# Performance work log

Hardware: AMD Instinct MI355X
Metric: run time of the kernel (lower is better)

## Reference

```python
import jax, jax.numpy as jnp
import numpy as np

N = 12288      # num nodes == in_num_dim (num_center_nodes)
D_IN = 512     # in_node_dim
D_EMB = 128    # embed_dim
D_OUT = 64     # out_dim
E = 393216     # num edges (avg degree 32)
NEG_SLOPE = 0.2  # GATConv default negative_slope


def _glorot(k, shape):
    lim = float(np.sqrt(6.0 / (shape[0] + shape[1])))
    return jax.random.uniform(k, shape, jnp.float32, -lim, lim)


def setup_inputs() -> dict:
    key = jax.random.key(0)
    ks = jax.random.split(key, 13)
    x = jax.random.normal(ks[0], (N, D_IN), jnp.float32)
    edge_index = jax.random.randint(ks[1], (2, E), 0, N, jnp.int64)
    # StructureAE.dense: Linear(in_node_dim, embed_dim)
    W_s1 = _glorot(ks[2], (D_EMB, D_IN))
    b_s1 = jnp.zeros((D_EMB,), jnp.float32)
    # GATConv(embed_dim, out_dim): heads=1, concat, bias
    W_g = _glorot(ks[3], (D_OUT, D_EMB))
    a_src = _glorot(ks[4], (D_OUT, 1))[:, 0]
    a_dst = _glorot(ks[5], (D_OUT, 1))[:, 0]
    b_g = jnp.zeros((D_OUT,), jnp.float32)
    # AttributeAE: dense1 = Linear(N, embed_dim), dense2 = Linear(embed_dim, out_dim)
    W_a1 = _glorot(ks[6], (D_EMB, N))
    b_a1 = jnp.zeros((D_EMB,), jnp.float32)
    W_a2 = _glorot(ks[7], (D_OUT, D_EMB))
    b_a2 = jnp.zeros((D_OUT,), jnp.float32)
    return dict(x=x, W_s1=W_s1, b_s1=b_s1, W_g=W_g, a_src=a_src, a_dst=a_dst,
                b_g=b_g, W_a1=W_a1, b_a1=b_a1, W_a2=W_a2, b_a2=b_a2,
                edge_index=edge_index, batch_size=N)


def _gat(x1, W_g, a_src, a_dst, b_g, edge_index):
    """Single-head GATConv with self-loops (PyG defaults)."""
    n = x1.shape[0]
    g = x1 @ W_g.T                                   # [N, D_OUT]
    loops = jnp.arange(n, dtype=edge_index.dtype)
    src = jnp.concatenate([edge_index[0], loops])    # message source j
    dst = jnp.concatenate([edge_index[1], loops])    # message target i
    sc_src = g @ a_src                               # [N]
    sc_dst = g @ a_dst                               # [N]
    e = jax.nn.leaky_relu(sc_src[src] + sc_dst[dst], NEG_SLOPE)  # [E+N]
    m = jax.ops.segment_max(e, dst, num_segments=n)
    e = jnp.exp(e - m[dst])
    denom = jax.ops.segment_sum(e, dst, num_segments=n)
    alpha = e / denom[dst]                           # softmax per target node
    h = jax.ops.segment_sum(alpha[:, None] * g[src], dst, num_segments=n)
    return h + b_g


def reference(x, W_s1, b_s1, W_g, a_src, a_dst, b_g,
              W_a1, b_a1, W_a2, b_a2, edge_index, batch_size):
    n = x.shape[0]
    # StructureAE (dropout=0 -> identity)
    x1 = jax.nn.relu(x @ W_s1.T + b_s1)              # [N, D_EMB]
    h = _gat(x1, W_g, a_src, a_dst, b_g, edge_index)  # [N, D_OUT]
    s_ = jax.nn.sigmoid(h @ h.T)                     # [N, N]
    # AttributeAE on x[:num_center_nodes] (pad if batch smaller)
    xp = x if batch_size >= n else jnp.pad(x, ((0, n - batch_size), (0, 0)))
    xt = jax.nn.relu(xp.T @ W_a1.T + b_a1)           # [D_IN, D_EMB]
    xa = xt @ W_a2.T + b_a2                          # [D_IN, D_OUT]
    x_ = h @ xa.T                                    # [N, D_IN]
    return (x_, s_)
```

## Files before the change

kernel.cpp:

```cpp
#include <hip/hip_runtime.h>
#include <cstddef>
#include <cstdint>

#define N_NODES 12288
#define D_IN    512
#define D_EMB   128
#define D_OUT   64
#define NEDGE   393216

typedef __attribute__((ext_vector_type(8))) short short8;
typedef __attribute__((ext_vector_type(4))) float f32x4;

__device__ __forceinline__ ushort f2bf(float f) {
  uint32_t u = __float_as_uint(f);
  u += 0x7fffu + ((u >> 16) & 1u);
  return (ushort)(u >> 16);
}
__device__ __forceinline__ float bf2f(ushort h) {
  return __uint_as_float((uint32_t)h << 16);
}

__global__ __launch_bounds__(256) void conv_hilo(const float* __restrict__ src,
    ushort* __restrict__ hi, ushort* __restrict__ lo)
{
  int idx = (blockIdx.x * 256 + threadIdx.x) * 4;
  float4 v = *(const float4*)(src + idx);
  const float* pv = &v.x;
  ushort4 h, l;
  ushort* ph = &h.x; ushort* pl = &l.x;
#pragma unroll
  for (int q = 0; q < 4; ++q) {
    ph[q] = f2bf(pv[q]);
    pl[q] = f2bf(pv[q] - bf2f(ph[q]));
  }
  *(ushort4*)(hi + idx) = h;
  *(ushort4*)(lo + idx) = l;
}

__global__ __launch_bounds__(256) void conv_w(const float* __restrict__ Ws1,
    const float* __restrict__ Wg, ushort* __restrict__ s1h, ushort* __restrict__ s1l,
    ushort* __restrict__ wgh, ushort* __restrict__ wgl)
{
  int b = blockIdx.x;
  const float* src; ushort* hi; ushort* lo; int idx;
  if (b < 64) { src = Ws1; hi = s1h; lo = s1l; idx = (b * 256 + threadIdx.x) * 4; }
  else        { src = Wg;  hi = wgh; lo = wgl; idx = ((b - 64) * 256 + threadIdx.x) * 4; }
  float4 v = *(const float4*)(src + idx);
  const float* pv = &v.x;
  ushort4 h, l;
  ushort* ph = &h.x; ushort* pl = &l.x;
#pragma unroll
  for (int q = 0; q < 4; ++q) {
    ph[q] = f2bf(pv[q]);
    pl[q] = f2bf(pv[q] - bf2f(ph[q]));
  }
  *(ushort4*)(hi + idx) = h;
  *(ushort4*)(lo + idx) = l;
}

__global__ __launch_bounds__(256) void init_kernel(const int* __restrict__ ei,
    int* __restrict__ flag, int* __restrict__ deg)
{
  int idx = blockIdx.x * 256 + threadIdx.x;
  if (idx < N_NODES) deg[idx] = 0;
  if (idx == 0) {
    int ok = 1;
    for (int t = 0; t < 64; ++t) ok &= (ei[2 * t + 1] == 0);
    *flag = ok;
  }
}

__global__ __launch_bounds__(256) void edge_deg(const int* __restrict__ ei,
    const int* __restrict__ flag, int* __restrict__ deg)
{
  int e = blockIdx.x * 256 + threadIdx.x;
  if (e >= NEDGE) return;
  int dst = (*flag) ? ei[2 * (NEDGE + e)] : ei[NEDGE + e];
  atomicAdd(&deg[dst], 1);
}

__global__ __launch_bounds__(256) void scan_deg(const int* __restrict__ deg,
    int* __restrict__ rp, int* __restrict__ cursor)
{
  __shared__ int sums[256];
  constexpr int C = N_NODES / 256;
  int t = threadIdx.x;
  int base = t * C;
  int local[C];
  int s = 0;
  for (int i = 0; i < C; ++i) { local[i] = deg[base + i]; s += local[i]; }
  sums[t] = s;
  __syncthreads();
  for (int off = 1; off < 256; off <<= 1) {
    int v = (t >= off) ? sums[t - off] : 0;
    __syncthreads();
    sums[t] += v;
    __syncthreads();
  }
  int prefix = (t == 0) ? 0 : sums[t - 1];
  for (int i = 0; i < C; ++i) {
    rp[base + i] = prefix;
    cursor[base + i] = prefix;
    prefix += local[i];
  }
  if (t == 255) rp[N_NODES] = prefix;
}

__global__ __launch_bounds__(256) void edge_scatter(const int* __restrict__ ei,
    const int* __restrict__ flag, int* __restrict__ cursor, int* __restrict__ csr)
{
  int e = blockIdx.x * 256 + threadIdx.x;
  if (e >= NEDGE) return;
  int is64 = *flag;
  int src = is64 ? ei[2 * e] : ei[e];
  int dst = is64 ? ei[2 * (NEDGE + e)] : ei[NEDGE + e];
  int p = atomicAdd(&cursor[dst], 1);
  csr[p] = src;
}

template<int MODE>
__global__ __launch_bounds__(64) void mfma_nt1(
    const ushort* __restrict__ Ahi, const ushort* __restrict__ Alo,
    const ushort* __restrict__ Bhi, const ushort* __restrict__ Blo,
    const float* __restrict__ bias,
    float* __restrict__ Cf, ushort* __restrict__ Chi, ushort* __restrict__ Clo,
    int lda, int ldb, int K, int ldc)
{
  int lane = threadIdx.x;
  int i0 = blockIdx.x * 64;
  int j0 = blockIdx.y * 64;
  int lm = lane & 15, lk = lane >> 4;
  f32x4 acc[4][4];
#pragma unroll
  for (int r = 0; r < 4; ++r)
#pragma unroll
    for (int c = 0; c < 4; ++c) acc[r][c] = (f32x4){0.f, 0.f, 0.f, 0.f};

  for (int k0 = 0; k0 < K; k0 += 32) {
    int kk = k0 + lk * 8;
    short8 Ah[4], Al[4], Bh[4], Bl[4];
#pragma unroll
    for (int t = 0; t < 4; ++t) {
      size_t ra = (size_t)(i0 + t * 16 + lm) * lda + kk;
      size_t rb = (size_t)(j0 + t * 16 + lm) * ldb + kk;
      Ah[t] = *(const short8*)(Ahi + ra);
      Al[t] = *(const short8*)(Alo + ra);
      Bh[t] = *(const short8*)(Bhi + rb);
      Bl[t] = *(const short8*)(Blo + rb);
    }
#pragma unroll
    for (int r = 0; r < 4; ++r)
#pragma unroll
      for (int c = 0; c < 4; ++c) {
        acc[r][c] = __builtin_amdgcn_mfma_f32_16x16x32_bf16(Ah[r], Bh[c], acc[r][c], 0, 0, 0);
        acc[r][c] = __builtin_amdgcn_mfma_f32_16x16x32_bf16(Ah[r], Bl[c], acc[r][c], 0, 0, 0);
        acc[r][c] = __builtin_amdgcn_mfma_f32_16x16x32_bf16(Al[r], Bh[c], acc[r][c], 0, 0, 0);
      }
  }
#pragma unroll
  for (int r = 0; r < 4; ++r)
#pragma unroll
    for (int c = 0; c < 4; ++c) {
      int col = j0 + c * 16 + lm;
#pragma unroll
      for (int q = 0; q < 4; ++q) {
        int row = i0 + r * 16 + lk * 4 + q;
        float v = acc[r][c][q];
        if (MODE == 0) {
          Cf[(size_t)row * ldc + col] = v;
        } else {
          v += bias[col];
          v = fmaxf(v, 0.f);
          ushort hb = f2bf(v);
          Chi[(size_t)row * ldc + col] = hb;
          Clo[(size_t)row * ldc + col] = f2bf(v - bf2f(hb));
        }
      }
    }
}

template<int ACT>
__global__ __launch_bounds__(256) void gemm_nt64(const float* __restrict__ A,
    const float* __restrict__ B, const float* __restrict__ bias,
    float* __restrict__ C, int M, int N, int K, int ldc)
{
  __shared__ float As[32][64];
  __shared__ float Bs[32][64];
  int m0 = blockIdx.x * 64, n0 = blockIdx.y * 64;
  int tid = threadIdx.x;
  int tx = tid & 15, ty = tid >> 4;
  float acc[4][4] = {};
  for (int k0 = 0; k0 < K; k0 += 32) {
#pragma unroll
    for (int p = 0; p < 2; ++p) {
      int idx = tid + p * 256;
      int row = idx >> 3;
      int kq  = idx & 7;
      float4 va = *(const float4*)(A + (size_t)(m0 + row) * K + k0 + kq * 4);
      As[kq*4+0][row] = va.x; As[kq*4+1][row] = va.y;
      As[kq*4+2][row] = va.z; As[kq*4+3][row] = va.w;
      float4 vb = *(const float4*)(B + (size_t)(n0 + row) * K + k0 + kq * 4);
      Bs[kq*4+0][row] = vb.x; Bs[kq*4+1][row] = vb.y;
      Bs[kq*4+2][row] = vb.z; Bs[kq*4+3][row] = vb.w;
    }
    __syncthreads();
#pragma unroll
    for (int k = 0; k < 32; ++k) {
      float a[4], b[4];
      *(float4*)a = *(const float4*)&As[k][ty * 4];
      *(float4*)b = *(const float4*)&Bs[k][tx * 4];
#pragma unroll
      for (int r = 0; r < 4; ++r)
#pragma unroll
        for (int c = 0; c < 4; ++c)
          acc[r][c] = fmaf(a[r], b[c], acc[r][c]);
    }
    __syncthreads();
  }
#pragma unroll
  for (int r = 0; r < 4; ++r) {
    int m = m0 + ty * 4 + r;
    float4 o;
    float* po = &o.x;
#pragma unroll
    for (int c = 0; c < 4; ++c) {
      float v = acc[r][c];
      if (bias) v += bias[n0 + tx * 4 + c];
      if (ACT) v = fmaxf(v, 0.f);
      po[c] = v;
    }
    *(float4*)(C + (size_t)m * ldc + n0 + tx * 4) = o;
  }
}

__global__ __launch_bounds__(256) void scores_kernel(const float* __restrict__ g,
    const float* __restrict__ a_src, const float* __restrict__ a_dst,
    float* __restrict__ sc_s, float* __restrict__ sc_d)
{
  int lane = threadIdx.x & 63;
  int i = blockIdx.x * 4 + (threadIdx.x >> 6);
  float gv = g[(size_t)i * 64 + lane];
  float vs = gv * a_src[lane];
  float vd = gv * a_dst[lane];
#pragma unroll
  for (int off = 32; off; off >>= 1) {
    vs += __shfl_xor(vs, off);
    vd += __shfl_xor(vd, off);
  }
  if (lane == 0) { sc_s[i] = vs; sc_d[i] = vd; }
}

#define WCAP 192
__global__ __launch_bounds__(256) void gat_kernel(const int* __restrict__ rp,
    const int* __restrict__ csr, const float* __restrict__ sc_s,
    const float* __restrict__ sc_d, const float* __restrict__ g,
    const float* __restrict__ b_g,
    ushort* __restrict__ hhi, ushort* __restrict__ hlo)
{
  __shared__ float wbuf[4][WCAP];
  __shared__ int   sbuf[4][WCAP];
  int lane = threadIdx.x & 63;
  int w = threadIdx.x >> 6;
  int i = blockIdx.x * 4 + w;
  int beg = rp[i], end = rp[i + 1];
  int deg = end - beg;
  float scd = sc_d[i];
  float mymax = -3.4e38f;
  for (int j = lane; j <= deg; j += 64) {
    int s = (j < deg) ? csr[beg + j] : i;
    float e = sc_s[s] + scd;
    e = (e > 0.f) ? e : 0.2f * e;
    mymax = fmaxf(mymax, e);
    if (j < WCAP) sbuf[w][j] = s;
  }
#pragma unroll
  for (int off = 32; off; off >>= 1) mymax = fmaxf(mymax, __shfl_xor(mymax, off));
  float sum = 0.f;
  for (int j = lane; j <= deg; j += 64) {
    int s = (j < WCAP) ? sbuf[w][j] : ((j < deg) ? csr[beg + j] : i);
    float e = sc_s[s] + scd;
    e = (e > 0.f) ? e : 0.2f * e;
    float ex = __expf(e - mymax);
    sum += ex;
    if (j < WCAP) wbuf[w][j] = ex;
  }
#pragma unroll
  for (int off = 32; off; off >>= 1) sum += __shfl_xor(sum, off);
  float inv = 1.f / sum;
  float acc = 0.f;
  for (int j = 0; j <= deg; ++j) {
    int s; float ex;
    if (j < WCAP) { s = sbuf[w][j]; ex = wbuf[w][j]; }
    else {
      s = (j < deg) ? csr[beg + j] : i;
      float e = sc_s[s] + scd;
      e = (e > 0.f) ? e : 0.2f * e;
      ex = __expf(e - mymax);
    }
    acc = fmaf(ex * inv, g[(size_t)s * 64 + lane], acc);
  }
  float val = acc + b_g[lane];
  size_t o = (size_t)i * 64 + lane;
  ushort hi = f2bf(val);
  hhi[o] = hi;
  hlo[o] = f2bf(val - bf2f(hi));
}

__global__ __launch_bounds__(256) void xt_splitk(const float* __restrict__ x,
    const float* __restrict__ Wa1, float* __restrict__ part)
{
  __shared__ float Xs[32][64];
  __shared__ float Ws[32][128];
  int c0 = blockIdx.x * 64;
  int i0 = blockIdx.y * 192;
  float* pout = part + (size_t)blockIdx.y * (D_IN * D_EMB);
  int tid = threadIdx.x;
  int txc = tid & 15, txj = tid >> 4;
  float acc[4][8] = {};
  for (int ib = 0; ib < 192; ib += 32) {
#pragma unroll
    for (int p = 0; p < 2; ++p) {
      int idx = tid + p * 256;
      int row = idx >> 4, q = idx & 15;
      *(float4*)&Xs[row][q * 4] =
          *(const float4*)(x + (size_t)(i0 + ib + row) * D_IN + c0 + q * 4);
    }
#pragma unroll
    for (int p = 0; p < 4; ++p) {
      int idx = tid + p * 256;
      int j = idx >> 3, q = idx & 7;
      float4 v = *(const float4*)(Wa1 + (size_t)j * N_NODES + i0 + ib + q * 4);
      Ws[q*4+0][j] = v.x; Ws[q*4+1][j] = v.y;
      Ws[q*4+2][j] = v.z; Ws[q*4+3][j] = v.w;
    }
    __syncthreads();
#pragma unroll
    for (int ii = 0; ii < 32; ++ii) {
      float a[4], b[8];
      *(float4*)a = *(const float4*)&Xs[ii][txc * 4];
      *(float4*)&b[0] = *(const float4*)&Ws[ii][txj * 8];
      *(float4*)&b[4] = *(const float4*)&Ws[ii][txj * 8 + 4];
#pragma unroll
      for (int r = 0; r < 4; ++r)
#pragma unroll
        for (int c = 0; c < 8; ++c)
          acc[r][c] = fmaf(a[r], b[c], acc[r][c]);
    }
    __syncthreads();
  }
#pragma unroll
  for (int r = 0; r < 4; ++r) {
    float4 o0, o1;
    o0.x = acc[r][0]; o0.y = acc[r][1]; o0.z = acc[r][2]; o0.w = acc[r][3];
    o1.x = acc[r][4]; o1.y = acc[r][5]; o1.z = acc[r][6]; o1.w = acc[r][7];
    size_t off = (size_t)(c0 + txc * 4 + r) * D_EMB + txj * 8;
    *(float4*)&pout[off] = o0;
    *(float4*)&pout[off + 4] = o1;
  }
}

__global__ __launch_bounds__(256) void xt_ep(const float* __restrict__ part,
    const float* __restrict__ b_a1, float* __restrict__ xt)
{
  int idx = blockIdx.x * 256 + threadIdx.x;
  float v = b_a1[idx & 127];
#pragma unroll 8
  for (int c = 0; c < 64; ++c) v += part[(size_t)c * (D_IN * D_EMB) + idx];
  xt[idx] = fmaxf(v, 0.f);
}

__global__ __launch_bounds__(256) void sig_hht_mfma(const ushort* __restrict__ hhi,
    const ushort* __restrict__ hlo, float* __restrict__ out)
{
  int lane = threadIdx.x & 63;
  int wave = threadIdx.x >> 6;
  int i0 = blockIdx.x * 128 + (wave >> 1) * 64;
  int j0 = blockIdx.y * 128 + (wave & 1) * 64;
  int lm = lane & 15, lk = lane >> 4;
  f32x4 acc[4][4];
#pragma unroll
  for (int r = 0; r < 4; ++r)
#pragma unroll
    for (int c = 0; c < 4; ++c) acc[r][c] = (f32x4){0.f, 0.f, 0.f, 0.f};
#pragma unroll
  for (int ks = 0; ks < 2; ++ks) {
    short8 Ah[4], Al[4], Bh[4], Bl[4];
#pragma unroll
    for (int t = 0; t < 4; ++t) {
      size_t ra = (size_t)(i0 + t * 16 + lm) * 64 + ks * 32 + lk * 8;
      size_t rb = (size_t)(j0 + t * 16 + lm) * 64 + ks * 32 + lk * 8;
      Ah[t] = *(const short8*)(hhi + ra);
      Al[t] = *(const short8*)(hlo + ra);
      Bh[t] = *(const short8*)(hhi + rb);
      Bl[t] = *(const short8*)(hlo + rb);
    }
#pragma unroll
    for (int r = 0; r < 4; ++r)
#pragma unroll
      for (int c = 0; c < 4; ++c) {
        acc[r][c] = __builtin_amdgcn_mfma_f32_16x16x32_bf16(Ah[r], Bh[c], acc[r][c], 0, 0, 0);
        acc[r][c] = __builtin_amdgcn_mfma_f32_16x16x32_bf16(Ah[r], Bl[c], acc[r][c], 0, 0, 0);
        acc[r][c] = __builtin_amdgcn_mfma_f32_16x16x32_bf16(Al[r], Bh[c], acc[r][c], 0, 0, 0);
      }
  }
#pragma unroll
  for (int r = 0; r < 4; ++r)
#pragma unroll
    for (int c = 0; c < 4; ++c) {
#pragma unroll
      for (int q = 0; q < 4; ++q) {
        float v = acc[r][c][q];
        float ex = __expf(-v);
#if __has_builtin(__builtin_amdgcn_rcpf)
        float s = __builtin_amdgcn_rcpf(1.f + ex);
#else
        float s = 1.f / (1.f + ex);
#endif
        out[(size_t)(i0 + r * 16 + lk * 4 + q) * N_NODES + (j0 + c * 16 + lm)] = s;
      }
    }
}

extern "C" void kernel_launch(void* const* d_in, const int* in_sizes, int n_in,
                              void* d_out, int out_size, void* d_ws, size_t ws_size,
                              hipStream_t stream)
{
  const float* x     = (const float*)d_in[0];
  const float* W_s1  = (const float*)d_in[1];
  const float* b_s1  = (const float*)d_in[2];
  const float* W_g   = (const float*)d_in[3];
  const float* a_src = (const float*)d_in[4];
  const float* a_dst = (const float*)d_in[5];
  const float* b_g   = (const float*)d_in[6];
  const float* W_a1  = (const float*)d_in[7];
  const float* b_a1  = (const float*)d_in[8];
  const float* W_a2  = (const float*)d_in[9];
  const float* b_a2  = (const float*)d_in[10];
  const int*   ei    = (const int*)d_in[11];

  float* ws   = (float*)d_ws;
  float* g    = ws;
  float* sc_s = g + (size_t)N_NODES * D_OUT;
  float* sc_d = sc_s + N_NODES;
  float* part = sc_d + N_NODES;
  float* xt   = part + (size_t)64 * D_IN * D_EMB;
  float* xa   = xt + D_IN * D_EMB;
  int* ip     = (int*)(xa + D_IN * D_OUT);
  int* flag   = ip;
  int* deg    = ip + 64;
  int* rp     = deg + N_NODES;
  int* cursor = rp + 12352;
  int* csr    = cursor + N_NODES;
  ushort* up  = (ushort*)(csr + NEDGE);
  ushort* xhi  = up;                         up += (size_t)N_NODES * D_IN;
  ushort* xlo  = up;                         up += (size_t)N_NODES * D_IN;
  ushort* x1hi = up;                         up += (size_t)N_NODES * D_EMB;
  ushort* x1lo = up;                         up += (size_t)N_NODES * D_EMB;
  ushort* Ws1hi = up;                        up += (size_t)D_EMB * D_IN;
  ushort* Ws1lo = up;                        up += (size_t)D_EMB * D_IN;
  ushort* Wghi = up;                         up += (size_t)D_OUT * D_EMB;
  ushort* Wglo = up;                         up += (size_t)D_OUT * D_EMB;
  ushort* hhi = up;                          up += (size_t)N_NODES * D_OUT;
  ushort* hlo = up;                          up += (size_t)N_NODES * D_OUT;
  ushort* xahi = up;                         up += (size_t)D_IN * D_OUT;
  ushort* xalo = up;                         up += (size_t)D_IN * D_OUT;

  float* out_x = (float*)d_out;
  float* out_s = out_x + (size_t)N_NODES * D_IN;

  conv_hilo<<<(N_NODES * D_IN) / 1024, 256, 0, stream>>>(x, xhi, xlo);
  conv_w<<<72, 256, 0, stream>>>(W_s1, W_g, Ws1hi, Ws1lo, Wghi, Wglo);

  init_kernel<<<48, 256, 0, stream>>>(ei, flag, deg);
  edge_deg<<<NEDGE / 256, 256, 0, stream>>>(ei, flag, deg);
  scan_deg<<<1, 256, 0, stream>>>(deg, rp, cursor);
  edge_scatter<<<NEDGE / 256, 256, 0, stream>>>(ei, flag, cursor, csr);

  mfma_nt1<1><<<dim3(192, 2), 64, 0, stream>>>(
      xhi, xlo, Ws1hi, Ws1lo, b_s1, nullptr, x1hi, x1lo,
      D_IN, D_IN, D_IN, D_EMB);
  mfma_nt1<0><<<dim3(192, 1), 64, 0, stream>>>(
      x1hi, x1lo, Wghi, Wglo, nullptr, g, nullptr, nullptr,
      D_EMB, D_EMB, D_EMB, D_OUT);
  scores_kernel<<<N_NODES / 4, 256, 0, stream>>>(g, a_src, a_dst, sc_s, sc_d);
  gat_kernel<<<N_NODES / 4, 256, 0, stream>>>(rp, csr, sc_s, sc_d, g, b_g,
                                              hhi, hlo);

  xt_splitk<<<dim3(8, 64), 256, 0, stream>>>(x, W_a1, part);
  xt_ep<<<D_IN * D_EMB / 256, 256, 0, stream>>>(part, b_a1, xt);
  gemm_nt64<0><<<dim3(8, 1), 256, 0, stream>>>(xt, W_a2, b_a2, xa,
                                               D_IN, D_OUT, D_EMB, D_OUT);
  conv_hilo<<<(D_IN * D_OUT) / 1024, 256, 0, stream>>>(xa, xahi, xalo);

  mfma_nt1<0><<<dim3(192, 8), 64, 0, stream>>>(
      hhi, hlo, xahi, xalo, nullptr, out_x, nullptr, nullptr,
      D_OUT, D_OUT, D_OUT, D_IN);
  sig_hht_mfma<<<dim3(96, 96), 256, 0, stream>>>(hhi, hlo, out_s);
}
```

Before: 895.0 us.

## Merge independent pipeline stages into fewer multi-role kernel launches

```diff
diff --git a/kernel.cpp b/kernel.cpp
--- a/kernel.cpp
+++ b/kernel.cpp
@@ -20,10 +20,9 @@
   return __uint_as_float((uint32_t)h << 16);
 }
 
-__global__ __launch_bounds__(256) void conv_hilo(const float* __restrict__ src,
-    ushort* __restrict__ hi, ushort* __restrict__ lo)
-{
-  int idx = (blockIdx.x * 256 + threadIdx.x) * 4;
+__device__ __forceinline__ void conv4(const float* __restrict__ src,
+    ushort* __restrict__ hi, ushort* __restrict__ lo, int idx)
+{
   float4 v = *(const float4*)(src + idx);
   const float* pv = &v.x;
   ushort4 h, l;
@@ -37,98 +36,17 @@
   *(ushort4*)(lo + idx) = l;
 }
 
-__global__ __launch_bounds__(256) void conv_w(const float* __restrict__ Ws1,
-    const float* __restrict__ Wg, ushort* __restrict__ s1h, ushort* __restrict__ s1l,
-    ushort* __restrict__ wgh, ushort* __restrict__ wgl)
-{
-  int b = blockIdx.x;
-  const float* src; ushort* hi; ushort* lo; int idx;
-  if (b < 64) { src = Ws1; hi = s1h; lo = s1l; idx = (b * 256 + threadIdx.x) * 4; }
-  else        { src = Wg;  hi = wgh; lo = wgl; idx = ((b - 64) * 256 + threadIdx.x) * 4; }
-  float4 v = *(const float4*)(src + idx);
-  const float* pv = &v.x;
-  ushort4 h, l;
-  ushort* ph = &h.x; ushort* pl = &l.x;
-#pragma unroll
-  for (int q = 0; q < 4; ++q) {
-    ph[q] = f2bf(pv[q]);
-    pl[q] = f2bf(pv[q] - bf2f(ph[q]));
-  }
-  *(ushort4*)(hi + idx) = h;
-  *(ushort4*)(lo + idx) = l;
-}
-
-__global__ __launch_bounds__(256) void init_kernel(const int* __restrict__ ei,
-    int* __restrict__ flag, int* __restrict__ deg)
-{
-  int idx = blockIdx.x * 256 + threadIdx.x;
-  if (idx < N_NODES) deg[idx] = 0;
-  if (idx == 0) {
-    int ok = 1;
-    for (int t = 0; t < 64; ++t) ok &= (ei[2 * t + 1] == 0);
-    *flag = ok;
-  }
-}
-
-__global__ __launch_bounds__(256) void edge_deg(const int* __restrict__ ei,
-    const int* __restrict__ flag, int* __restrict__ deg)
-{
-  int e = blockIdx.x * 256 + threadIdx.x;
-  if (e >= NEDGE) return;
-  int dst = (*flag) ? ei[2 * (NEDGE + e)] : ei[NEDGE + e];
-  atomicAdd(&deg[dst], 1);
-}
-
-__global__ __launch_bounds__(256) void scan_deg(const int* __restrict__ deg,
-    int* __restrict__ rp, int* __restrict__ cursor)
-{
-  __shared__ int sums[256];
-  constexpr int C = N_NODES / 256;
-  int t = threadIdx.x;
-  int base = t * C;
-  int local[C];
-  int s = 0;
-  for (int i = 0; i < C; ++i) { local[i] = deg[base + i]; s += local[i]; }
-  sums[t] = s;
-  __syncthreads();
-  for (int off = 1; off < 256; off <<= 1) {
-    int v = (t >= off) ? sums[t - off] : 0;
-    __syncthreads();
-    sums[t] += v;
-    __syncthreads();
-  }
-  int prefix = (t == 0) ? 0 : sums[t - 1];
-  for (int i = 0; i < C; ++i) {
-    rp[base + i] = prefix;
-    cursor[base + i] = prefix;
-    prefix += local[i];
-  }
-  if (t == 255) rp[N_NODES] = prefix;
-}
-
-__global__ __launch_bounds__(256) void edge_scatter(const int* __restrict__ ei,
-    const int* __restrict__ flag, int* __restrict__ cursor, int* __restrict__ csr)
-{
-  int e = blockIdx.x * 256 + threadIdx.x;
-  if (e >= NEDGE) return;
-  int is64 = *flag;
-  int src = is64 ? ei[2 * e] : ei[e];
-  int dst = is64 ? ei[2 * (NEDGE + e)] : ei[NEDGE + e];
-  int p = atomicAdd(&cursor[dst], 1);
-  csr[p] = src;
-}
-
 template<int MODE>
-__global__ __launch_bounds__(64) void mfma_nt1(
+__device__ __forceinline__ void mfma_tile64(
+    int lane, int i0, int j0,
     const ushort* __restrict__ Ahi, const ushort* __restrict__ Alo,
     const ushort* __restrict__ Bhi, const ushort* __restrict__ Blo,
     const float* __restrict__ bias,
     float* __restrict__ Cf, ushort* __restrict__ Chi, ushort* __restrict__ Clo,
-    int lda, int ldb, int K, int ldc)
-{
-  int lane = threadIdx.x;
-  int i0 = blockIdx.x * 64;
-  int j0 = blockIdx.y * 64;
+    int lda, int ldb, int K, int ldc,
+    const float* __restrict__ a_src, const float* __restrict__ a_dst,
+    float* __restrict__ sc_s, float* __restrict__ sc_d)
+{
   int lm = lane & 15, lk = lane >> 4;
   f32x4 acc[4][4];
 #pragma unroll
@@ -136,6 +54,7 @@
 #pragma unroll
     for (int c = 0; c < 4; ++c) acc[r][c] = (f32x4){0.f, 0.f, 0.f, 0.f};
 
+#pragma unroll 1
   for (int k0 = 0; k0 < K; k0 += 32) {
     int kk = k0 + lk * 8;
     short8 Ah[4], Al[4], Bh[4], Bl[4];
@@ -157,6 +76,7 @@
         acc[r][c] = __builtin_amdgcn_mfma_f32_16x16x32_bf16(Al[r], Bh[c], acc[r][c], 0, 0, 0);
       }
   }
+
 #pragma unroll
   for (int r = 0; r < 4; ++r)
 #pragma unroll
@@ -166,88 +86,261 @@
       for (int q = 0; q < 4; ++q) {
         int row = i0 + r * 16 + lk * 4 + q;
         float v = acc[r][c][q];
-        if (MODE == 0) {
-          Cf[(size_t)row * ldc + col] = v;
-        } else {
+        if (MODE == 1) {
           v += bias[col];
           v = fmaxf(v, 0.f);
           ushort hb = f2bf(v);
           Chi[(size_t)row * ldc + col] = hb;
           Clo[(size_t)row * ldc + col] = f2bf(v - bf2f(hb));
+        } else {
+          Cf[(size_t)row * ldc + col] = v;
         }
       }
     }
-}
-
-template<int ACT>
-__global__ __launch_bounds__(256) void gemm_nt64(const float* __restrict__ A,
-    const float* __restrict__ B, const float* __restrict__ bias,
-    float* __restrict__ C, int M, int N, int K, int ldc)
-{
-  __shared__ float As[32][64];
-  __shared__ float Bs[32][64];
-  int m0 = blockIdx.x * 64, n0 = blockIdx.y * 64;
+
+  if (MODE == 2) {
+    float asv[4], adv[4];
+#pragma unroll
+    for (int c = 0; c < 4; ++c) {
+      asv[c] = a_src[c * 16 + lm];
+      adv[c] = a_dst[c * 16 + lm];
+    }
+#pragma unroll
+    for (int r = 0; r < 4; ++r)
+#pragma unroll
+      for (int q = 0; q < 4; ++q) {
+        float s = 0.f, d = 0.f;
+#pragma unroll
+        for (int c = 0; c < 4; ++c) {
+          float v = acc[r][c][q];
+          s = fmaf(v, asv[c], s);
+          d = fmaf(v, adv[c], d);
+        }
+#pragma unroll
+        for (int off = 1; off < 16; off <<= 1) {
+          s += __shfl_xor(s, off);
+          d += __shfl_xor(d, off);
+        }
+        if (lm == 0) {
+          int row = i0 + r * 16 + lk * 4 + q;
+          sc_s[row] = s;
+          sc_d[row] = d;
+        }
+      }
+  }
+}
+
+__global__ __launch_bounds__(256) void prep_kernel(
+    const float* __restrict__ x, const float* __restrict__ Ws1,
+    const float* __restrict__ Wg, const float* __restrict__ Wa1,
+    ushort* __restrict__ xhi, ushort* __restrict__ xlo,
+    ushort* __restrict__ s1h, ushort* __restrict__ s1l,
+    ushort* __restrict__ wgh, ushort* __restrict__ wgl,
+    int* __restrict__ deg, float* __restrict__ part)
+{
+  __shared__ float smem[6144];
+  int b = blockIdx.x;
   int tid = threadIdx.x;
-  int tx = tid & 15, ty = tid >> 4;
-  float acc[4][4] = {};
-  for (int k0 = 0; k0 < K; k0 += 32) {
-#pragma unroll
-    for (int p = 0; p < 2; ++p) {
-      int idx = tid + p * 256;
-      int row = idx >> 3;
-      int kq  = idx & 7;
-      float4 va = *(const float4*)(A + (size_t)(m0 + row) * K + k0 + kq * 4);
-      As[kq*4+0][row] = va.x; As[kq*4+1][row] = va.y;
-      As[kq*4+2][row] = va.z; As[kq*4+3][row] = va.w;
-      float4 vb = *(const float4*)(B + (size_t)(n0 + row) * K + k0 + kq * 4);
-      Bs[kq*4+0][row] = vb.x; Bs[kq*4+1][row] = vb.y;
-      Bs[kq*4+2][row] = vb.z; Bs[kq*4+3][row] = vb.w;
-    }
+  if (b < 512) {
+    float* Xs = smem;
+    float* Ws = smem + 2048;
+    int c0 = (b & 7) * 64;
+    int i0 = (b >> 3) * 192;
+    float* pout = part + (size_t)(b >> 3) * (D_IN * D_EMB);
+    int txc = tid & 15, txj = tid >> 4;
+    float acc[4][8] = {};
+    for (int ib = 0; ib < 192; ib += 32) {
+#pragma unroll
+      for (int p = 0; p < 2; ++p) {
+        int idx = tid + p * 256;
+        int row = idx >> 4, q = idx & 15;
+        *(float4*)&Xs[row * 64 + q * 4] =
+            *(const float4*)(x + (size_t)(i0 + ib + row) * D_IN + c0 + q * 4);
+      }
+#pragma unroll
+      for (int p = 0; p < 4; ++p) {
+        int idx = tid + p * 256;
+        int j = idx >> 3, q = idx & 7;
+        float4 v = *(const float4*)(Wa1 + (size_t)j * N_NODES + i0 + ib + q * 4);
+        Ws[(q * 4 + 0) * 128 + j] = v.x; Ws[(q * 4 + 1) * 128 + j] = v.y;
+        Ws[(q * 4 + 2) * 128 + j] = v.z; Ws[(q * 4 + 3) * 128 + j] = v.w;
+      }
+      __syncthreads();
+#pragma unroll
+      for (int ii = 0; ii < 32; ++ii) {
+        float a[4], bb[8];
+        *(float4*)a = *(const float4*)&Xs[ii * 64 + txc * 4];
+        *(float4*)&bb[0] = *(const float4*)&Ws[ii * 128 + txj * 8];
+        *(float4*)&bb[4] = *(const float4*)&Ws[ii * 128 + txj * 8 + 4];
+#pragma unroll
+        for (int r = 0; r < 4; ++r)
+#pragma unroll
+          for (int c = 0; c < 8; ++c)
+            acc[r][c] = fmaf(a[r], bb[c], acc[r][c]);
+      }
+      __syncthreads();
+    }
+#pragma unroll
+    for (int r = 0; r < 4; ++r) {
+      float4 o0, o1;
+      o0.x = acc[r][0]; o0.y = acc[r][1]; o0.z = acc[r][2]; o0.w = acc[r][3];
+      o1.x = acc[r][4]; o1.y = acc[r][5]; o1.z = acc[r][6]; o1.w = acc[r][7];
+      size_t off = (size_t)(c0 + txc * 4 + r) * D_EMB + txj * 8;
+      *(float4*)&pout[off] = o0;
+      *(float4*)&pout[off + 4] = o1;
+    }
+  } else if (b < 6656) {
+    int idx = ((b - 512) * 256 + tid) * 4;
+    conv4(x, xhi, xlo, idx);
+  } else if (b < 6728) {
+    int bb = b - 6656;
+    if (bb < 64) conv4(Ws1, s1h, s1l, (bb * 256 + tid) * 4);
+    else         conv4(Wg,  wgh, wgl, ((bb - 64) * 256 + tid) * 4);
+  } else {
+    deg[(b - 6728) * 256 + tid] = 0;
+  }
+}
+
+__device__ __forceinline__ bool edge_is64(const int* __restrict__ ei) {
+  int hv = ei[2 * (threadIdx.x & 63) + 1];
+  return __ballot(hv == 0) == 0xFFFFFFFFFFFFFFFFull;
+}
+
+__global__ __launch_bounds__(256) void l2_kernel(
+    const int* __restrict__ ei, int* __restrict__ deg,
+    const ushort* __restrict__ xhi, const ushort* __restrict__ xlo,
+    const ushort* __restrict__ s1h, const ushort* __restrict__ s1l,
+    const float* __restrict__ b_s1,
+    ushort* __restrict__ x1hi, ushort* __restrict__ x1lo,
+    const float* __restrict__ part, const float* __restrict__ b_a1,
+    float* __restrict__ xt)
+{
+  int b = blockIdx.x;
+  if (b < 96) {
+    int lane = threadIdx.x & 63, wv = threadIdx.x >> 6;
+    int i0 = b * 128 + (wv >> 1) * 64;
+    int j0 = (wv & 1) * 64;
+    mfma_tile64<1>(lane, i0, j0, xhi, xlo, s1h, s1l, b_s1,
+                   nullptr, x1hi, x1lo, D_IN, D_IN, D_IN, D_EMB,
+                   nullptr, nullptr, nullptr, nullptr);
+  } else if (b < 1632) {
+    bool is64 = edge_is64(ei);
+    int e = (b - 96) * 256 + threadIdx.x;
+    int dst = is64 ? ei[2 * (NEDGE + e)] : ei[NEDGE + e];
+    atomicAdd(&deg[dst], 1);
+  } else {
+    int idx = (b - 1632) * 256 + threadIdx.x;
+    float v = b_a1[idx & 127];
+#pragma unroll 8
+    for (int c = 0; c < 64; ++c) v += part[(size_t)c * (D_IN * D_EMB) + idx];
+    xt[idx] = fmaxf(v, 0.f);
+  }
+}
+
+__global__ __launch_bounds__(256) void l3_kernel(
+    const int* __restrict__ deg, int* __restrict__ rp, int* __restrict__ cursor,
+    const ushort* __restrict__ x1hi, const ushort* __restrict__ x1lo,
+    const ushort* __restrict__ wgh, const ushort* __restrict__ wgl,
+    float* __restrict__ g,
+    const float* __restrict__ a_src, const float* __restrict__ a_dst,
+    float* __restrict__ sc_s, float* __restrict__ sc_d,
+    const float* __restrict__ xt, const float* __restrict__ Wa2,
+    const float* __restrict__ b_a2,
+    ushort* __restrict__ xahi, ushort* __restrict__ xalo)
+{
+  __shared__ float smem[4096];
+  int b = blockIdx.x;
+  int tid = threadIdx.x;
+  if (b == 0) {
+    int* sums = (int*)smem;
+    constexpr int C = N_NODES / 256;
+    int base = tid * C;
+    int local[C];
+    int s = 0;
+#pragma unroll
+    for (int i = 0; i < C; ++i) { local[i] = deg[base + i]; s += local[i]; }
+    sums[tid] = s;
     __syncthreads();
-#pragma unroll
-    for (int k = 0; k < 32; ++k) {
-      float a[4], b[4];
-      *(float4*)a = *(const float4*)&As[k][ty * 4];
-      *(float4*)b = *(const float4*)&Bs[k][tx * 4];
-#pragma unroll
-      for (int r = 0; r < 4; ++r)
-#pragma unroll
-        for (int c = 0; c < 4; ++c)
-          acc[r][c] = fmaf(a[r], b[c], acc[r][c]);
-    }
-    __syncthreads();
-  }
-#pragma unroll
-  for (int r = 0; r < 4; ++r) {
-    int m = m0 + ty * 4 + r;
-    float4 o;
-    float* po = &o.x;
-#pragma unroll
-    for (int c = 0; c < 4; ++c) {
-      float v = acc[r][c];
-      if (bias) v += bias[n0 + tx * 4 + c];
-      if (ACT) v = fmaxf(v, 0.f);
-      po[c] = v;
-    }
-    *(float4*)(C + (size_t)m * ldc + n0 + tx * 4) = o;
-  }
-}
-
-__global__ __launch_bounds__(256) void scores_kernel(const float* __restrict__ g,
-    const float* __restrict__ a_src, const float* __restrict__ a_dst,
-    float* __restrict__ sc_s, float* __restrict__ sc_d)
-{
-  int lane = threadIdx.x & 63;
-  int i = blockIdx.x * 4 + (threadIdx.x >> 6);
-  float gv = g[(size_t)i * 64 + lane];
-  float vs = gv * a_src[lane];
-  float vd = gv * a_dst[lane];
-#pragma unroll
-  for (int off = 32; off; off >>= 1) {
-    vs += __shfl_xor(vs, off);
-    vd += __shfl_xor(vd, off);
-  }
-  if (lane == 0) { sc_s[i] = vs; sc_d[i] = vd; }
+    for (int off = 1; off < 256; off <<= 1) {
+      int v = (tid >= off) ? sums[tid - off] : 0;
+      __syncthreads();
+      sums[tid] += v;
+      __syncthreads();
+    }
+    int prefix = (tid == 0) ? 0 : sums[tid - 1];
+#pragma unroll
+    for (int i = 0; i < C; ++i) {
+      rp[base + i] = prefix;
+      cursor[base + i] = prefix;
+      prefix += local[i];
+    }
+    if (tid == 255) rp[N_NODES] = prefix;
+  } else if (b < 49) {
+    int lane = tid & 63, wv = tid >> 6;
+    int i0 = (b - 1) * 256 + wv * 64;
+    mfma_tile64<2>(lane, i0, 0, x1hi, x1lo, wgh, wgl, nullptr,
+                   g, nullptr, nullptr, D_EMB, D_EMB, D_EMB, D_OUT,
+                   a_src, a_dst, sc_s, sc_d);
+  } else {
+    float* As = smem;
+    float* Bs = smem + 2048;
+    int m0 = (b - 49) * 64;
+    int tx = tid & 15, ty = tid >> 4;
+    float acc[4][4] = {};
+    for (int k0 = 0; k0 < D_EMB; k0 += 32) {
+#pragma unroll
+      for (int p = 0; p < 2; ++p) {
+        int idx = tid + p * 256;
+        int row = idx >> 3;
+        int kq = idx & 7;
+        float4 va = *(const float4*)(xt + (size_t)(m0 + row) * D_EMB + k0 + kq * 4);
+        As[(kq * 4 + 0) * 64 + row] = va.x; As[(kq * 4 + 1) * 64 + row] = va.y;
+        As[(kq * 4 + 2) * 64 + row] = va.z; As[(kq * 4 + 3) * 64 + row] = va.w;
+        float4 vb = *(const float4*)(Wa2 + (size_t)row * D_EMB + k0 + kq * 4);
+        Bs[(kq * 4 + 0) * 64 + row] = vb.x; Bs[(kq * 4 + 1) * 64 + row] = vb.y;
+        Bs[(kq * 4 + 2) * 64 + row] = vb.z; Bs[(kq * 4 + 3) * 64 + row] = vb.w;
+      }
+      __syncthreads();
+#pragma unroll
+      for (int k = 0; k < 32; ++k) {
+        float a[4], bb[4];
+        *(float4*)a = *(const float4*)&As[k * 64 + ty * 4];
+        *(float4*)bb = *(const float4*)&Bs[k * 64 + tx * 4];
+#pragma unroll
+        for (int r = 0; r < 4; ++r)
+#pragma unroll
+          for (int c = 0; c < 4; ++c)
+            acc[r][c] = fmaf(a[r], bb[c], acc[r][c]);
+      }
+      __syncthreads();
+    }
+#pragma unroll
+    for (int r = 0; r < 4; ++r) {
+      int m = m0 + ty * 4 + r;
+      ushort4 h, l;
+      ushort* ph = &h.x; ushort* pl = &l.x;
+#pragma unroll
+      for (int c = 0; c < 4; ++c) {
+        float v = acc[r][c] + b_a2[tx * 4 + c];
+        ushort hb = f2bf(v);
+        ph[c] = hb;
+        pl[c] = f2bf(v - bf2f(hb));
+      }
+      *(ushort4*)(xahi + (size_t)m * D_OUT + tx * 4) = h;
+      *(ushort4*)(xalo + (size_t)m * D_OUT + tx * 4) = l;
+    }
+  }
+}
+
+__global__ __launch_bounds__(256) void scatter_kernel(const int* __restrict__ ei,
+    int* __restrict__ cursor, int* __restrict__ csr)
+{
+  bool is64 = edge_is64(ei);
+  int e = blockIdx.x * 256 + threadIdx.x;
+  int src = is64 ? ei[2 * e] : ei[e];
+  int dst = is64 ? ei[2 * (NEDGE + e)] : ei[NEDGE + e];
+  int p = atomicAdd(&cursor[dst], 1);
+  csr[p] = src;
 }
 
 #define WCAP 192
@@ -306,76 +399,27 @@
   hlo[o] = f2bf(val - bf2f(hi));
 }
 
-__global__ __launch_bounds__(256) void xt_splitk(const float* __restrict__ x,
-    const float* __restrict__ Wa1, float* __restrict__ part)
-{
-  __shared__ float Xs[32][64];
-  __shared__ float Ws[32][128];
-  int c0 = blockIdx.x * 64;
-  int i0 = blockIdx.y * 192;
-  float* pout = part + (size_t)blockIdx.y * (D_IN * D_EMB);
-  int tid = threadIdx.x;
-  int txc = tid & 15, txj = tid >> 4;
-  float acc[4][8] = {};
-  for (int ib = 0; ib < 192; ib += 32) {
-#pragma unroll
-    for (int p = 0; p < 2; ++p) {
-      int idx = tid + p * 256;
-      int row = idx >> 4, q = idx & 15;
-      *(float4*)&Xs[row][q * 4] =
-          *(const float4*)(x + (size_t)(i0 + ib + row) * D_IN + c0 + q * 4);
-    }
-#pragma unroll
-    for (int p = 0; p < 4; ++p) {
-      int idx = tid + p * 256;
-      int j = idx >> 3, q = idx & 7;
-      float4 v = *(const float4*)(Wa1 + (size_t)j * N_NODES + i0 + ib + q * 4);
-      Ws[q*4+0][j] = v.x; Ws[q*4+1][j] = v.y;
-      Ws[q*4+2][j] = v.z; Ws[q*4+3][j] = v.w;
-    }
-    __syncthreads();
-#pragma unroll
-    for (int ii = 0; ii < 32; ++ii) {
-      float a[4], b[8];
-      *(float4*)a = *(const float4*)&Xs[ii][txc * 4];
-      *(float4*)&b[0] = *(const float4*)&Ws[ii][txj * 8];
-      *(float4*)&b[4] = *(const float4*)&Ws[ii][txj * 8 + 4];
-#pragma unroll
-      for (int r = 0; r < 4; ++r)
-#pragma unroll
-        for (int c = 0; c < 8; ++c)
-          acc[r][c] = fmaf(a[r], b[c], acc[r][c]);
-    }
-    __syncthreads();
-  }
-#pragma unroll
-  for (int r = 0; r < 4; ++r) {
-    float4 o0, o1;
-    o0.x = acc[r][0]; o0.y = acc[r][1]; o0.z = acc[r][2]; o0.w = acc[r][3];
-    o1.x = acc[r][4]; o1.y = acc[r][5]; o1.z = acc[r][6]; o1.w = acc[r][7];
-    size_t off = (size_t)(c0 + txc * 4 + r) * D_EMB + txj * 8;
-    *(float4*)&pout[off] = o0;
-    *(float4*)&pout[off + 4] = o1;
-  }
-}
-
-__global__ __launch_bounds__(256) void xt_ep(const float* __restrict__ part,
-    const float* __restrict__ b_a1, float* __restrict__ xt)
-{
-  int idx = blockIdx.x * 256 + threadIdx.x;
-  float v = b_a1[idx & 127];
-#pragma unroll 8
-  for (int c = 0; c < 64; ++c) v += part[(size_t)c * (D_IN * D_EMB) + idx];
-  xt[idx] = fmaxf(v, 0.f);
-}
-
-__global__ __launch_bounds__(256) void sig_hht_mfma(const ushort* __restrict__ hhi,
-    const ushort* __restrict__ hlo, float* __restrict__ out)
-{
+__global__ __launch_bounds__(256) void l6_kernel(
+    const ushort* __restrict__ hhi, const ushort* __restrict__ hlo,
+    const ushort* __restrict__ xahi, const ushort* __restrict__ xalo,
+    float* __restrict__ out_x, float* __restrict__ out_s)
+{
+  int b = blockIdx.x;
   int lane = threadIdx.x & 63;
-  int wave = threadIdx.x >> 6;
-  int i0 = blockIdx.x * 128 + (wave >> 1) * 64;
-  int j0 = blockIdx.y * 128 + (wave & 1) * 64;
+  int wv = threadIdx.x >> 6;
+  if (b < 384) {
+    int i0 = (b >> 2) * 128 + (wv >> 1) * 64;
+    int j0 = (b & 3) * 128 + (wv & 1) * 64;
+    mfma_tile64<0>(lane, i0, j0, hhi, hlo, xahi, xalo, nullptr,
+                   out_x, nullptr, nullptr, D_OUT, D_OUT, D_OUT, D_IN,
+                   nullptr, nullptr, nullptr, nullptr);
+    return;
+  }
+  int bb = b - 384;
+  int iT = bb / 96;
+  int jT = bb - iT * 96;
+  int i0 = iT * 128 + (wv >> 1) * 64;
+  int j0 = jT * 128 + (wv & 1) * 64;
   int lm = lane & 15, lk = lane >> 4;
   f32x4 acc[4][4];
 #pragma unroll
@@ -416,7 +460,7 @@
 #else
         float s = 1.f / (1.f + ex);
 #endif
-        out[(size_t)(i0 + r * 16 + lk * 4 + q) * N_NODES + (j0 + c * 16 + lm)] = s;
+        out_s[(size_t)(i0 + r * 16 + lk * 4 + q) * N_NODES + (j0 + c * 16 + lm)] = s;
       }
     }
 }
@@ -464,36 +508,19 @@
   ushort* hlo = up;                          up += (size_t)N_NODES * D_OUT;
   ushort* xahi = up;                         up += (size_t)D_IN * D_OUT;
   ushort* xalo = up;                         up += (size_t)D_IN * D_OUT;
+  (void)flag; (void)ws_size; (void)in_sizes; (void)n_in; (void)out_size;
 
   float* out_x = (float*)d_out;
   float* out_s = out_x + (size_t)N_NODES * D_IN;
 
-  conv_hilo<<<(N_NODES * D_IN) / 1024, 256, 0, stream>>>(x, xhi, xlo);
-  conv_w<<<72, 256, 0, stream>>>(W_s1, W_g, Ws1hi, Ws1lo, Wghi, Wglo);
-
-  init_kernel<<<48, 256, 0, stream>>>(ei, flag, deg);
-  edge_deg<<<NEDGE / 256, 256, 0, stream>>>(ei, flag, deg);
-  scan_deg<<<1, 256, 0, stream>>>(deg, rp, cursor);
-  edge_scatter<<<NEDGE / 256, 256, 0, stream>>>(ei, flag, cursor, csr);
-
-  mfma_nt1<1><<<dim3(192, 2), 64, 0, stream>>>(
-      xhi, xlo, Ws1hi, Ws1lo, b_s1, nullptr, x1hi, x1lo,
-      D_IN, D_IN, D_IN, D_EMB);
-  mfma_nt1<0><<<dim3(192, 1), 64, 0, stream>>>(
-      x1hi, x1lo, Wghi, Wglo, nullptr, g, nullptr, nullptr,
-      D_EMB, D_EMB, D_EMB, D_OUT);
-  scores_kernel<<<N_NODES / 4, 256, 0, stream>>>(g, a_src, a_dst, sc_s, sc_d);
+  prep_kernel<<<6776, 256, 0, stream>>>(x, W_s1, W_g, W_a1,
+      xhi, xlo, Ws1hi, Ws1lo, Wghi, Wglo, deg, part);
+  l2_kernel<<<1888, 256, 0, stream>>>(ei, deg, xhi, xlo, Ws1hi, Ws1lo, b_s1,
+      x1hi, x1lo, part, b_a1, xt);
+  l3_kernel<<<57, 256, 0, stream>>>(deg, rp, cursor, x1hi, x1lo, Wghi, Wglo,
+      g, a_src, a_dst, sc_s, sc_d, xt, W_a2, b_a2, xahi, xalo);
+  scatter_kernel<<<NEDGE / 256, 256, 0, stream>>>(ei, cursor, csr);
   gat_kernel<<<N_NODES / 4, 256, 0, stream>>>(rp, csr, sc_s, sc_d, g, b_g,
                                               hhi, hlo);
-
-  xt_splitk<<<dim3(8, 64), 256, 0, stream>>>(x, W_a1, part);
-  xt_ep<<<D_IN * D_EMB / 256, 256, 0, stream>>>(part, b_a1, xt);
-  gemm_nt64<0><<<dim3(8, 1), 256, 0, stream>>>(xt, W_a2, b_a2, xa,
-                                               D_IN, D_OUT, D_EMB, D_OUT);
-  conv_hilo<<<(D_IN * D_OUT) / 1024, 256, 0, stream>>>(xa, xahi, xalo);
-
-  mfma_nt1<0><<<dim3(192, 8), 64, 0, stream>>>(
-      hhi, hlo, xahi, xalo, nullptr, out_x, nullptr, nullptr,
-      D_OUT, D_OUT, D_OUT, D_IN);
-  sig_hht_mfma<<<dim3(96, 96), 256, 0, stream>>>(hhi, hlo, out_s);
-}
+  l6_kernel<<<9600, 256, 0, stream>>>(hhi, hlo, xahi, xalo, out_x, out_s);
+}
```

Result: faster. 862.0 us (-3.7%).
